# Optimization experiments

Measured on AMD Instinct MI355X. Metric: run time of the kernel, lower is better.

The kernel has to match this reference:

```python
import jax, jax.numpy as jnp
import numpy as np

N_QKV = 64
N_EMBED = 2048
B = 4
T = 2048  # must equal N_EMBED because the module's causal mask is n_embed x n_embed


def setup_inputs() -> dict:
    key = jax.random.key(0)
    ks = jax.random.split(key, 7)
    s = 1.0 / np.sqrt(N_EMBED)
    return {
        "x": jax.random.normal(ks[0], (B, T, N_EMBED), dtype=jnp.float32),
        "Wq": jax.random.normal(ks[1], (N_QKV, N_EMBED), dtype=jnp.float32) * s,
        "bq": jnp.zeros((N_QKV,), dtype=jnp.float32),
        "Wk": jax.random.normal(ks[2], (N_QKV, N_EMBED), dtype=jnp.float32) * s,
        "bk": jnp.zeros((N_QKV,), dtype=jnp.float32),
        "Wv": jax.random.normal(ks[3], (N_QKV, N_EMBED), dtype=jnp.float32) * s,
        "bv": jnp.zeros((N_QKV,), dtype=jnp.float32),
    }


def reference(x, Wq, bq, Wk, bk, Wv, bv):
    # Linear projections: torch nn.Linear computes x @ W.T + b
    q = jnp.einsum("bte,qe->btq", x, Wq) + bq  # [B, T, n_qkv]
    k = jnp.einsum("bte,qe->btq", x, Wk) + bk
    v = jnp.einsum("bte,qe->btq", x, Wv) + bv
    scale = 1.0 / jnp.sqrt(jnp.asarray(N_QKV, dtype=x.dtype))
    logits = jnp.einsum("btq,bsq->bts", q, k) * scale  # [B, T, T]
    # causal mask: upper triangle (strictly above diagonal) -> -inf
    causal = jnp.tril(jnp.ones((T, T), dtype=bool))
    logits = jnp.where(causal, logits, jnp.asarray(-jnp.inf, dtype=logits.dtype))
    probs = jax.nn.softmax(logits, axis=-1)
    return jnp.einsum("bts,bsq->btq", probs, v)  # [B, T, n_qkv]
```

## Files before the change

kernel.cpp:

```cpp
#include <hip/hip_runtime.h>
#include <hip/hip_bf16.h>

#define T_SEQ 2048
#define E_DIM 2048
#define D_HEAD 64
#define B_SZ 4
#define NROWS (B_SZ * T_SEQ)

typedef __attribute__((ext_vector_type(8))) short bf16x8;
typedef __attribute__((ext_vector_type(4))) float f32x4;
typedef __attribute__((ext_vector_type(4))) unsigned short u16x4;
typedef __attribute__((ext_vector_type(8))) unsigned short u16x8;

__device__ __forceinline__ unsigned short f2bf(float x) {
    __hip_bfloat16 h = __float2bfloat16(x);
    return *reinterpret_cast<unsigned short*>(&h);
}

__device__ __forceinline__ u16x8 cvt8(float4 a, float4 b) {
    u16x8 t;
    t[0] = f2bf(a.x); t[1] = f2bf(a.y); t[2] = f2bf(a.z); t[3] = f2bf(a.w);
    t[4] = f2bf(b.x); t[5] = f2bf(b.y); t[6] = f2bf(b.z); t[7] = f2bf(b.w);
    return t;
}

__device__ __forceinline__ bf16x8 cvtfrag2(f32x4 lo, f32x4 hi) {
    bf16x8 f;
    #pragma unroll
    for (int j = 0; j < 4; ++j) {
        f[j]     = (short)f2bf(lo[j]);
        f[4 + j] = (short)f2bf(hi[j]);
    }
    return f;
}

__device__ __forceinline__ bf16x8 ldfrag(const unsigned short* p) {
    u16x4 lo = *(const u16x4*)p;
    u16x4 hi = *(const u16x4*)(p + 16);
    bf16x8 f;
    #pragma unroll
    for (int j = 0; j < 4; ++j) { f[j] = (short)lo[j]; f[4 + j] = (short)hi[j]; }
    return f;
}

__device__ __forceinline__ void lds_fence_barrier() {
    asm volatile("s_waitcnt lgkmcnt(0)" ::: "memory");
    __builtin_amdgcn_s_barrier();
}

__device__ __forceinline__ void gl_lds16(const void* gsrc, void* ldst) {
    __builtin_amdgcn_global_load_lds(
        (const __attribute__((address_space(1))) unsigned int*)(unsigned long long)gsrc,
        (__attribute__((address_space(3))) unsigned int*)(unsigned long long)ldst,
        16, 0, 0);
}

__global__ __launch_bounds__(256) void wcvt_kernel(
    const float* __restrict__ Wq, const float* __restrict__ Wk,
    const float* __restrict__ Wv, unsigned short* __restrict__ Wp)
{
    const int gid = blockIdx.x * 256 + threadIdx.x;
    const int l    = gid & 63;
    const int k32  = (gid >> 6) & 63;
    const int f    = gid >> 12;
    const int r    = l & 15;
    const int g    = l >> 4;
    const int n    = 16 * f + r;
    const int pj   = n >> 6;
    const int o    = n & 63;
    const float* __restrict__ src = (pj == 0) ? Wq : (pj == 1) ? Wk : Wv;
    const float* p = src + (size_t)o * E_DIM + k32 * 32 + g * 4;
    float4 a = *(const float4*)p;
    float4 b = *(const float4*)(p + 16);
    *(u16x8*)(Wp + (size_t)gid * 8) = cvt8(a, b);
}

__global__ __launch_bounds__(512) void proj_mfma_kernel(
    const float* __restrict__ x, const unsigned short* __restrict__ Wp,
    const float* __restrict__ bq, const float* __restrict__ bk,
    const float* __restrict__ bv,
    __hip_bfloat16* __restrict__ qb, __hip_bfloat16* __restrict__ kb,
    __hip_bfloat16* __restrict__ vb)
{
    __shared__ unsigned char lds[4][32768];

    const int tid  = threadIdx.x;
    const int w    = tid >> 6;
    const int l    = tid & 63;
    const int r    = l & 15;
    const int g    = l >> 4;
    const int wm   = w >> 2;
    const int wn   = w & 3;
    const int row0 = blockIdx.x * 32;
    const int phase = blockIdx.x & 31;

    const int xrow = tid >> 4;
    const int xjl  = (tid & 15) ^ (xrow & 7);
    const unsigned char* xsrc =
        (const unsigned char*)(x + (size_t)(row0 + xrow) * E_DIM + xjl * 4);
    const int xdst = tid * 16;
    const unsigned char* wsrc[3];
    int wdst[3];
    #pragma unroll
    for (int i = 0; i < 3; ++i) {
        const int cw = tid + i * 512;
        const int f  = cw >> 7;
        const int kc = (cw >> 6) & 1;
        const int lw = cw & 63;
        wsrc[i] = (const unsigned char*)Wp + (size_t)(f * 64 + kc) * 1024 + lw * 16;
        wdst[i] = 8192 + cw * 16;
    }

    f32x4 acc[3];
    #pragma unroll
    for (int ff = 0; ff < 3; ++ff) acc[ff] = (f32x4){0.f, 0.f, 0.f, 0.f};

    auto stage = [&](int tt, int bi) {
        gl_lds16(xsrc + (size_t)tt * 256, &lds[bi][xdst]);
        #pragma unroll
        for (int i = 0; i < 3; ++i)
            gl_lds16(wsrc[i] + (size_t)tt * 2048, &lds[bi][wdst[i]]);
    };

    const int arow  = wm * 16 + r;
    const int amask = arow & 7;
    const int abase = arow * 256;

    auto compute = [&](int bi) {
        bf16x8 af[2];
        #pragma unroll
        for (int kk = 0; kk < 2; ++kk) {
            f32x4 lo = *(const f32x4*)&lds[bi][abase + (((kk * 8 + g)     ^ amask) * 16)];
            f32x4 hi = *(const f32x4*)&lds[bi][abase + (((kk * 8 + 4 + g) ^ amask) * 16)];
            af[kk] = cvtfrag2(lo, hi);
        }
        #pragma unroll
        for (int ff = 0; ff < 3; ++ff) {
            const int f = wn * 3 + ff;
            #pragma unroll
            for (int kk = 0; kk < 2; ++kk) {
                bf16x8 bfm = *(const bf16x8*)&lds[bi][8192 + ((f * 2 + kk) * 64 + l) * 16];
                acc[ff] = __builtin_amdgcn_mfma_f32_16x16x32_bf16(af[kk], bfm, acc[ff], 0, 0, 0);
            }
        }
    };

    stage((0 + phase) & 31, 0);
    stage((1 + phase) & 31, 1);
    stage((2 + phase) & 31, 2);
    asm volatile("s_waitcnt vmcnt(8)" ::: "memory");
    __builtin_amdgcn_s_barrier();

    for (int t = 0; t < 29; ++t) {
        stage((t + 3 + phase) & 31, (t + 3) & 3);
        compute(t & 3);
        asm volatile("s_waitcnt vmcnt(8)" ::: "memory");
        __builtin_amdgcn_s_barrier();
    }
    compute(29 & 3);
    asm volatile("s_waitcnt vmcnt(4)" ::: "memory");
    __builtin_amdgcn_s_barrier();
    compute(30 & 3);
    asm volatile("s_waitcnt vmcnt(0)" ::: "memory");
    __builtin_amdgcn_s_barrier();
    compute(31 & 3);

    #pragma unroll
    for (int ff = 0; ff < 3; ++ff) {
        const int f  = wn * 3 + ff;
        const int n  = 16 * f + r;
        const int pj = n >> 6;
        const int o  = n & 63;
        const float* bias = (pj == 0) ? bq : (pj == 1) ? bk : bv;
        __hip_bfloat16* dst = (pj == 0) ? qb : (pj == 1) ? kb : vb;
        const float scale = (pj == 0) ? 0.18033688011112042f : 1.0f;
        const float bv_ = bias[o];
        #pragma unroll
        for (int j = 0; j < 4; ++j) {
            const int row = row0 + wm * 16 + 4 * g + j;
            dst[(size_t)row * D_HEAD + o] =
                __float2bfloat16((acc[ff][j] + bv_) * scale);
        }
    }
}

#define LDK 72
#define LDV 68
#define LDP 68

__global__ __launch_bounds__(128) void attn_part_kernel(
    const __hip_bfloat16* __restrict__ qg, const __hip_bfloat16* __restrict__ kg,
    const __hip_bfloat16* __restrict__ vg, float* __restrict__ Op,
    float* __restrict__ Ml, int tpc, int nch)
{
    const int qt = blockIdx.x;
    const int ch = blockIdx.y;
    const int total64 = qt / 2 + 1;
    if (ch * tpc >= total64) return;

    __shared__ unsigned short Kl[64 * LDK];
    __shared__ unsigned short Vt[64 * LDV];
    __shared__ unsigned short Pl[2 * 16 * LDP];

    const int tid = threadIdx.x;
    const int w   = tid >> 6;
    const int l   = tid & 63;
    const int r   = l & 15;
    const int g   = l >> 4;
    const int q0  = qt * 32;
    const int b   = blockIdx.z;
    const size_t base = (size_t)b * T_SEQ;

    const unsigned short* qb16 = (const unsigned short*)qg;
    const unsigned short* kb16 = (const unsigned short*)kg;
    const unsigned short* vb16 = (const unsigned short*)vg;

    const unsigned short* qrow = qb16 + (base + q0 + 16 * w + r) * D_HEAD;
    bf16x8 qf[2];
    #pragma unroll
    for (int kk = 0; kk < 2; ++kk)
        qf[kk] = ldfrag(qrow + 32 * kk + 4 * g);

    f32x4 acc_o[4];
    #pragma unroll
    for (int dn = 0; dn < 4; ++dn) acc_o[dn] = (f32x4){0.f, 0.f, 0.f, 0.f};
    float m4[4] = {-1e30f, -1e30f, -1e30f, -1e30f};
    float l4[4] = {0.f, 0.f, 0.f, 0.f};

    unsigned short* pw = &Pl[w * 16 * LDP];
    const int ntiles = min(tpc, total64 - ch * tpc);
    const int y = tid & 15, z = tid >> 4;
    const int s0base = ch * tpc * 64;

    u16x8 kr[4];
    u16x4 va4[4], vb4[4];

    auto issue = [&](int s0) {
        #pragma unroll
        for (int i = 0; i < 4; ++i) {
            const int c = tid + i * 128;
            kr[i] = *(const u16x8*)(kb16 + (base + s0 + (c >> 3)) * D_HEAD + (c & 7) * 8);
        }
        #pragma unroll
        for (int m = 0; m < 4; ++m) {
            const int sl = 2 * (z + 8 * m);
            const int d0 = y * 4;
            va4[m] = *(const u16x4*)(vb16 + (base + s0 + sl) * D_HEAD + d0);
            vb4[m] = *(const u16x4*)(vb16 + (base + s0 + sl + 1) * D_HEAD + d0);
        }
    };

    issue(s0base);

    for (int it = 0; it < ntiles; ++it) {
        const int s0 = s0base + it * 64;

        __builtin_amdgcn_s_barrier();

        #pragma unroll
        for (int i = 0; i < 4; ++i) {
            const int c = tid + i * 128;
            *(u16x8*)(&Kl[(c >> 3) * LDK + (c & 7) * 8]) = kr[i];
        }
        #pragma unroll
        for (int m = 0; m < 4; ++m) {
            const int sl = 2 * (z + 8 * m);
            const int d0 = y * 4;
            #pragma unroll
            for (int i = 0; i < 4; ++i) {
                unsigned int pr = (unsigned int)(unsigned short)va4[m][i] |
                                  ((unsigned int)(unsigned short)vb4[m][i] << 16);
                *(unsigned int*)&Vt[(d0 + i) * LDV + sl] = pr;
            }
        }
        lds_fence_barrier();

        if (it + 1 < ntiles) issue(s0 + 64);

        f32x4 s_acc[4];
        #pragma unroll
        for (int nt = 0; nt < 4; ++nt) s_acc[nt] = (f32x4){0.f, 0.f, 0.f, 0.f};
        __builtin_amdgcn_s_setprio(1);
        #pragma unroll
        for (int nt = 0; nt < 4; ++nt)
            #pragma unroll
            for (int kk = 0; kk < 2; ++kk) {
                bf16x8 bf = ldfrag(&Kl[(nt * 16 + r) * LDK + kk * 32 + 4 * g]);
                s_acc[nt] = __builtin_amdgcn_mfma_f32_16x16x32_bf16(qf[kk], bf, s_acc[nt], 0, 0, 0);
            }
        __builtin_amdgcn_s_setprio(0);

        if (s0 + 64 > q0) {
            #pragma unroll
            for (int nt = 0; nt < 4; ++nt)
                #pragma unroll
                for (int j = 0; j < 4; ++j)
                    if (s0 + nt * 16 + r > q0 + 16 * w + 4 * g + j)
                        s_acc[nt][j] = -1e30f;
        }

        float tm[4];
        #pragma unroll
        for (int j = 0; j < 4; ++j)
            tm[j] = fmaxf(fmaxf(s_acc[0][j], s_acc[1][j]),
                          fmaxf(s_acc[2][j], s_acc[3][j]));
        #pragma unroll
        for (int mask = 1; mask < 16; mask <<= 1)
            #pragma unroll
            for (int j = 0; j < 4; ++j)
                tm[j] = fmaxf(tm[j], __shfl_xor(tm[j], mask));

        float p[4][4], rs[4];
        #pragma unroll
        for (int j = 0; j < 4; ++j) {
            const float mn = fmaxf(m4[j], tm[j]);
            const float sc = exp2f(m4[j] - mn);
            m4[j] = mn;
            rs[j] = 0.f;
            #pragma unroll
            for (int nt = 0; nt < 4; ++nt) {
                p[nt][j] = exp2f(s_acc[nt][j] - mn);
                rs[j] += p[nt][j];
            }
            l4[j] *= sc;
            acc_o[0][j] *= sc; acc_o[1][j] *= sc;
            acc_o[2][j] *= sc; acc_o[3][j] *= sc;
        }
        #pragma unroll
        for (int mask = 1; mask < 16; mask <<= 1)
            #pragma unroll
            for (int j = 0; j < 4; ++j)
                rs[j] += __shfl_xor(rs[j], mask);
        #pragma unroll
        for (int j = 0; j < 4; ++j) l4[j] += rs[j];

        #pragma unroll
        for (int nt = 0; nt < 4; ++nt)
            #pragma unroll
            for (int j = 0; j < 4; ++j)
                pw[(4 * g + j) * LDP + nt * 16 + r] = f2bf(p[nt][j]);

        bf16x8 pf[2];
        #pragma unroll
        for (int kk = 0; kk < 2; ++kk)
            pf[kk] = ldfrag(&pw[r * LDP + kk * 32 + 4 * g]);

        __builtin_amdgcn_s_setprio(1);
        #pragma unroll
        for (int dn = 0; dn < 4; ++dn)
            #pragma unroll
            for (int kk = 0; kk < 2; ++kk) {
                bf16x8 vf = ldfrag(&Vt[(dn * 16 + r) * LDV + kk * 32 + 4 * g]);
                acc_o[dn] = __builtin_amdgcn_mfma_f32_16x16x32_bf16(pf[kk], vf, acc_o[dn], 0, 0, 0);
            }
        __builtin_amdgcn_s_setprio(0);
    }

    const size_t pidx = ((size_t)(b * 64 + qt) * nch + ch);
    float* op = Op + pidx * 2048;
    #pragma unroll
    for (int j = 0; j < 4; ++j) {
        const int row = 16 * w + 4 * g + j;
        #pragma unroll
        for (int dn = 0; dn < 4; ++dn)
            op[row * 64 + dn * 16 + r] = acc_o[dn][j];
        if (r == 0) {
            Ml[pidx * 64 + row]      = m4[j];
            Ml[pidx * 64 + 32 + row] = l4[j];
        }
    }
}

__global__ __launch_bounds__(256) void attn_combine_kernel(
    const float* __restrict__ Op, const float* __restrict__ Ml,
    float* __restrict__ out, int tpc, int nch)
{
    const int qt = blockIdx.x;
    const int b  = blockIdx.y;
    const int total64 = qt / 2 + 1;
    const int nact = (total64 + tpc - 1) / tpc;
    const size_t pbase = (size_t)(b * 64 + qt) * nch;

    __shared__ float wgt[8][32];
    __shared__ float linv[32];

    const int tid = threadIdx.x;
    if (tid < 32) {
        float M = -1e30f;
        for (int c = 0; c < nact; ++c)
            M = fmaxf(M, Ml[(pbase + c) * 64 + tid]);
        float L = 0.f;
        for (int c = 0; c < nact; ++c) {
            float wv = exp2f(Ml[(pbase + c) * 64 + tid] - M);
            wgt[c][tid] = wv;
            L += wv * Ml[(pbase + c) * 64 + 32 + tid];
        }
        linv[tid] = 1.0f / L;
    }
    __syncthreads();

    const int d  = tid & 63;
    const int r0 = tid >> 6;
    for (int row = r0; row < 32; row += 4) {
        float a = 0.f;
        for (int c = 0; c < nact; ++c)
            a += wgt[c][row] * Op[(pbase + c) * 2048 + row * 64 + d];
        out[((size_t)b * T_SEQ + qt * 32 + row) * D_HEAD + d] = a * linv[row];
    }
}

extern "C" void kernel_launch(void* const* d_in, const int* in_sizes, int n_in,
                              void* d_out, int out_size, void* d_ws, size_t ws_size,
                              hipStream_t stream) {
    const float* x  = (const float*)d_in[0];
    const float* Wq = (const float*)d_in[1];
    const float* bq = (const float*)d_in[2];
    const float* Wk = (const float*)d_in[3];
    const float* bk = (const float*)d_in[4];
    const float* Wv = (const float*)d_in[5];
    const float* bv = (const float*)d_in[6];
    float* out = (float*)d_out;

    __hip_bfloat16* qb = (__hip_bfloat16*)d_ws;
    __hip_bfloat16* kb = qb + (size_t)NROWS * D_HEAD;
    __hip_bfloat16* vb = kb + (size_t)NROWS * D_HEAD;
    unsigned short* Wp = (unsigned short*)(vb + (size_t)NROWS * D_HEAD);
    float* Op = (float*)((char*)d_ws + (4u << 20));

    int nch = 8;
    while (nch > 1 &&
           (4u << 20) + (size_t)256 * nch * (2048 + 64) * 4 > ws_size)
        nch >>= 1;
    const int tpc = 32 / nch;
    float* Ml = Op + (size_t)256 * nch * 2048;

    wcvt_kernel<<<192, 256, 0, stream>>>(Wq, Wk, Wv, Wp);
    proj_mfma_kernel<<<NROWS / 32, 512, 0, stream>>>(x, Wp, bq, bk, bv, qb, kb, vb);
    attn_part_kernel<<<dim3(64, nch, B_SZ), 128, 0, stream>>>(qb, kb, vb, Op, Ml, tpc, nch);
    attn_combine_kernel<<<dim3(64, B_SZ), 256, 0, stream>>>(Op, Ml, out, tpc, nch);
}
```

Baseline: 64.04 us.

## Pre-convert x to bf16 in MFMA fragment layout in a separate kernel

Adds an xcvt kernel that converts the fp32 activations into bf16, packed in the exact MFMA A-fragment order, and writes them to workspace. The projection kernel then stages the already-converted fragments into LDS with half the threads, so it no longer does per-fragment fp32-to-bf16 conversion or swizzled fp32 LDS reads. The LDS footprint shrinks and the vmcnt waits are split per wave group. In exchange it adds an extra kernel launch plus a full write and re-read of a 32 MB bf16 copy of x, which raises total memory traffic for a bandwidth-bound stage.

```diff
diff --git a/kernel.cpp b/kernel.cpp
--- a/kernel.cpp
+++ b/kernel.cpp
@@ -22,16 +22,6 @@
     t[0] = f2bf(a.x); t[1] = f2bf(a.y); t[2] = f2bf(a.z); t[3] = f2bf(a.w);
     t[4] = f2bf(b.x); t[5] = f2bf(b.y); t[6] = f2bf(b.z); t[7] = f2bf(b.w);
     return t;
-}
-
-__device__ __forceinline__ bf16x8 cvtfrag2(f32x4 lo, f32x4 hi) {
-    bf16x8 f;
-    #pragma unroll
-    for (int j = 0; j < 4; ++j) {
-        f[j]     = (short)f2bf(lo[j]);
-        f[4 + j] = (short)f2bf(hi[j]);
-    }
-    return f;
 }
 
 __device__ __forceinline__ bf16x8 ldfrag(const unsigned short* p) {
@@ -75,14 +65,34 @@
     *(u16x8*)(Wp + (size_t)gid * 8) = cvt8(a, b);
 }
 
+__global__ __launch_bounds__(256) void xcvt_kernel(
+    const float* __restrict__ x, unsigned short* __restrict__ Xp)
+{
+    const int b   = blockIdx.x;
+    const int tid = threadIdx.x;
+    const int kt  = b & 31;
+    const int rt  = b >> 5;
+    const int sub = tid >> 6;
+    const int l   = tid & 63;
+    const int wm  = sub >> 1;
+    const int kk  = sub & 1;
+    const int r   = l & 15;
+    const int g   = l >> 4;
+    const float* p = x + (size_t)(rt * 32 + wm * 16 + r) * E_DIM
+                       + kt * 64 + kk * 32 + 4 * g;
+    float4 lo = *(const float4*)p;
+    float4 hi = *(const float4*)(p + 16);
+    *(u16x8*)(Xp + ((size_t)b * 256 + tid) * 8) = cvt8(lo, hi);
+}
+
 __global__ __launch_bounds__(512) void proj_mfma_kernel(
-    const float* __restrict__ x, const unsigned short* __restrict__ Wp,
+    const unsigned short* __restrict__ Xp, const unsigned short* __restrict__ Wp,
     const float* __restrict__ bq, const float* __restrict__ bk,
     const float* __restrict__ bv,
     __hip_bfloat16* __restrict__ qb, __hip_bfloat16* __restrict__ kb,
     __hip_bfloat16* __restrict__ vb)
 {
-    __shared__ unsigned char lds[4][32768];
+    __shared__ unsigned char lds[4][28672];
 
     const int tid  = threadIdx.x;
     const int w    = tid >> 6;
@@ -94,11 +104,8 @@
     const int row0 = blockIdx.x * 32;
     const int phase = blockIdx.x & 31;
 
-    const int xrow = tid >> 4;
-    const int xjl  = (tid & 15) ^ (xrow & 7);
-    const unsigned char* xsrc =
-        (const unsigned char*)(x + (size_t)(row0 + xrow) * E_DIM + xjl * 4);
-    const int xdst = tid * 16;
+    const unsigned char* xbase =
+        (const unsigned char*)Xp + (size_t)blockIdx.x * 131072;
     const unsigned char* wsrc[3];
     int wdst[3];
     #pragma unroll
@@ -108,7 +115,7 @@
         const int kc = (cw >> 6) & 1;
         const int lw = cw & 63;
         wsrc[i] = (const unsigned char*)Wp + (size_t)(f * 64 + kc) * 1024 + lw * 16;
-        wdst[i] = 8192 + cw * 16;
+        wdst[i] = 4096 + cw * 16;
     }
 
     f32x4 acc[3];
@@ -116,49 +123,48 @@
     for (int ff = 0; ff < 3; ++ff) acc[ff] = (f32x4){0.f, 0.f, 0.f, 0.f};
 
     auto stage = [&](int tt, int bi) {
-        gl_lds16(xsrc + (size_t)tt * 256, &lds[bi][xdst]);
+        if (tid < 256)
+            gl_lds16(xbase + (size_t)tt * 4096 + tid * 16, &lds[bi][tid * 16]);
         #pragma unroll
         for (int i = 0; i < 3; ++i)
             gl_lds16(wsrc[i] + (size_t)tt * 2048, &lds[bi][wdst[i]]);
     };
 
-    const int arow  = wm * 16 + r;
-    const int amask = arow & 7;
-    const int abase = arow * 256;
-
     auto compute = [&](int bi) {
         bf16x8 af[2];
         #pragma unroll
-        for (int kk = 0; kk < 2; ++kk) {
-            f32x4 lo = *(const f32x4*)&lds[bi][abase + (((kk * 8 + g)     ^ amask) * 16)];
-            f32x4 hi = *(const f32x4*)&lds[bi][abase + (((kk * 8 + 4 + g) ^ amask) * 16)];
-            af[kk] = cvtfrag2(lo, hi);
-        }
+        for (int kk = 0; kk < 2; ++kk)
+            af[kk] = *(const bf16x8*)&lds[bi][((wm * 2 + kk) * 64 + l) * 16];
         #pragma unroll
         for (int ff = 0; ff < 3; ++ff) {
             const int f = wn * 3 + ff;
             #pragma unroll
             for (int kk = 0; kk < 2; ++kk) {
-                bf16x8 bfm = *(const bf16x8*)&lds[bi][8192 + ((f * 2 + kk) * 64 + l) * 16];
+                bf16x8 bfm = *(const bf16x8*)&lds[bi][4096 + ((f * 2 + kk) * 64 + l) * 16];
                 acc[ff] = __builtin_amdgcn_mfma_f32_16x16x32_bf16(af[kk], bfm, acc[ff], 0, 0, 0);
             }
         }
+    };
+
+    auto wait_steady = [&]() {
+        if (w < 4) asm volatile("s_waitcnt vmcnt(8)" ::: "memory");
+        else       asm volatile("s_waitcnt vmcnt(6)" ::: "memory");
+        __builtin_amdgcn_s_barrier();
     };
 
     stage((0 + phase) & 31, 0);
     stage((1 + phase) & 31, 1);
     stage((2 + phase) & 31, 2);
-    asm volatile("s_waitcnt vmcnt(8)" ::: "memory");
-    __builtin_amdgcn_s_barrier();
+    wait_steady();
 
     for (int t = 0; t < 29; ++t) {
         stage((t + 3 + phase) & 31, (t + 3) & 3);
         compute(t & 3);
-        asm volatile("s_waitcnt vmcnt(8)" ::: "memory");
-        __builtin_amdgcn_s_barrier();
+        wait_steady();
     }
     compute(29 & 3);
-    asm volatile("s_waitcnt vmcnt(4)" ::: "memory");
+    if (w < 4) asm volatile("s_waitcnt vmcnt(4)" ::: "memory");
+    else       asm volatile("s_waitcnt vmcnt(3)" ::: "memory");
     __builtin_amdgcn_s_barrier();
     compute(30 & 3);
     asm volatile("s_waitcnt vmcnt(0)" ::: "memory");
@@ -426,16 +432,18 @@
     __hip_bfloat16* vb = kb + (size_t)NROWS * D_HEAD;
     unsigned short* Wp = (unsigned short*)(vb + (size_t)NROWS * D_HEAD);
     float* Op = (float*)((char*)d_ws + (4u << 20));
+    unsigned short* Xp = (unsigned short*)((char*)d_ws + (24u << 20));
 
     int nch = 8;
     while (nch > 1 &&
-           (4u << 20) + (size_t)256 * nch * (2048 + 64) * 4 > ws_size)
+           (24u << 20) + (size_t)NROWS * E_DIM * 2 > ws_size)
         nch >>= 1;
     const int tpc = 32 / nch;
     float* Ml = Op + (size_t)256 * nch * 2048;
 
     wcvt_kernel<<<192, 256, 0, stream>>>(Wq, Wk, Wv, Wp);
-    proj_mfma_kernel<<<NROWS / 32, 512, 0, stream>>>(x, Wp, bq, bk, bv, qb, kb, vb);
+    xcvt_kernel<<<NROWS / 32 * 32, 256, 0, stream>>>(x, Xp);
+    proj_mfma_kernel<<<NROWS / 32, 512, 0, stream>>>(Xp, Wp, bq, bk, bv, qb, kb, vb);
     attn_part_kernel<<<dim3(64, nch, B_SZ), 128, 0, stream>>>(qb, kb, vb, Op, Ml, tpc, nch);
     attn_combine_kernel<<<dim3(64, B_SZ), 256, 0, stream>>>(Op, Ml, out, tpc, nch);
 }
```

Result: slower. 76.71 us (+19.8%).
